# Kernel tuning notes

Hardware: AMD Instinct MI355X
Metric: run time of the kernel (lower is better)

The kernel has to match this reference:

```python
import jax, jax.numpy as jnp
import numpy as np

VOCAB = 30000
FEAT = 30000
HID = 1024
EMB = 1024
B, LQ, LKV = 32, 256, 256


def setup_inputs() -> dict:
    key = jax.random.key(0)
    ks = jax.random.split(key, 8)
    captions = jax.random.randint(ks[0], (B, LKV), 0, VOCAB)
    targets_feature = jax.random.randint(ks[1], (B, LKV), 0, FEAT)
    hidden_state = jax.random.normal(ks[2], (B, LQ, HID), dtype=jnp.float32)
    feature_mask = jax.random.uniform(ks[3], (B, LQ, LKV), dtype=jnp.float32)
    # embeddings initialized uniform(-0.1, 0.1) per init_weights
    Wa = jax.random.uniform(ks[4], (VOCAB, HID), minval=-0.1, maxval=0.1, dtype=jnp.float32)
    Wc = jax.random.uniform(ks[5], (FEAT, HID), minval=-0.1, maxval=0.1, dtype=jnp.float32)
    r = np.sqrt(6.0) / np.sqrt(2 * HID + EMB)
    fc_w = jax.random.uniform(ks[6], (EMB, 2 * HID), minval=-r, maxval=r, dtype=jnp.float32)
    fc_b = jnp.zeros((EMB,), dtype=jnp.float32)
    return {"captions": captions, "hidden_state": hidden_state,
            "targets_feature": targets_feature, "feature_mask": feature_mask,
            "Wa": Wa, "Wc": Wc, "fc_w": fc_w, "fc_b": fc_b}


def reference(captions, hidden_state, targets_feature, feature_mask, Wa, Wc, fc_w, fc_b):
    ea = Wa[captions]           # [B, LKV, H]
    ec = Wc[targets_feature]    # [B, LKV, H]
    # u = hidden_state @ embedding_a^T : [B, LQ, LKV]
    u = jnp.einsum('bqh,bkh->bqk', hidden_state, ea)
    mask = jnp.clip(feature_mask, 0.0, 1.0)
    delta = jnp.exp(u) * mask
    p = delta / (jnp.sum(delta, axis=2, keepdims=True) + 1e-10)  # masked softmax-like weights
    # weighted value sum without materializing [B,LQ,LKV,H] broadcasts
    o = jnp.einsum('bqk,bkh->bqh', p, ec)
    o = jnp.concatenate([hidden_state, o], axis=2)               # [B, LQ, 2H]
    o = o @ fc_w.T + fc_b                                        # [B, LQ, EMB]
    o = o + 1e-10
    norm = jnp.sqrt(jnp.sum(o * o, axis=-1, keepdims=True)) + 1e-8
    return o / norm
```

## Files before the change

### kernel.cpp

```cpp
#include <hip/hip_runtime.h>
#include <hip/hip_bf16.h>

typedef __attribute__((ext_vector_type(8))) short short8;
typedef __attribute__((ext_vector_type(4))) float f32x4;
using bf16 = __hip_bfloat16;


__device__ __forceinline__ void glds16(const void* g, void* lds) {
  __builtin_amdgcn_global_load_lds(
      (const __attribute__((address_space(1))) void*)g,
      (__attribute__((address_space(3))) void*)lds, 16, 0, 0);
}

__global__ __launch_bounds__(256) void k1_prep(
    const int* __restrict__ captions, const float* __restrict__ Wa,
    const float* __restrict__ H, const float* __restrict__ fcw,
    const int* __restrict__ targets, const float* __restrict__ Wc,
    bf16* __restrict__ EA, bf16* __restrict__ X, bf16* __restrict__ FW,
    bf16* __restrict__ ECT) {
  __shared__ float T[64][67];
  int task = blockIdx.x;
  int tid = threadIdx.x;
  if (task < 17408) {
    const float* src;
    bf16* dst;
    int n;
    if (task < 8192) {
      src = Wa + (size_t)captions[task] * 1024;
      dst = EA + (size_t)task * 1024;
      n = 1024;
    } else if (task < 16384) {
      int t = task - 8192;
      src = H + (size_t)t * 1024;
      dst = X + (size_t)t * 2048;
      n = 1024;
    } else {
      int t = task - 16384;
      src = fcw + (size_t)t * 2048;
      dst = FW + (size_t)t * 2048;
      n = 2048;
    }
    for (int c = tid * 4; c < n; c += 1024) {
      float4 v = *(const float4*)(src + c);
      __hip_bfloat162 p0, p1;
      p0.x = __float2bfloat16(v.x); p0.y = __float2bfloat16(v.y);
      p1.x = __float2bfloat16(v.z); p1.y = __float2bfloat16(v.w);
      *(__hip_bfloat162*)(dst + c) = p0;
      *(__hip_bfloat162*)(dst + c + 2) = p1;
    }
    return;
  }
  int bid = task - 17408;
  int b = bid >> 6;
  int kt = (bid >> 4) & 3;
  int ht = bid & 15;
#pragma unroll
  for (int p = 0; p < 4; ++p) {
    int k = p * 16 + (tid >> 4);
    int idx = targets[b * 256 + kt * 64 + k];
    const float* s = Wc + (size_t)idx * 1024 + ht * 64 + (tid & 15) * 4;
    float4 v = *(const float4*)s;
    int c = (tid & 15) * 4;
    T[k][c] = v.x; T[k][c + 1] = v.y; T[k][c + 2] = v.z; T[k][c + 3] = v.w;
  }
  __syncthreads();
#pragma unroll
  for (int p = 0; p < 8; ++p) {
    int h = p * 8 + (tid >> 5);
    int k = (tid & 31) * 2;
    __hip_bfloat162 o;
    o.x = __float2bfloat16(T[k][h]);
    o.y = __float2bfloat16(T[k + 1][h]);
    *(__hip_bfloat162*)(ECT + ((size_t)b * 1024 + ht * 64 + h) * 256 + kt * 64 + k) = o;
  }
}

__global__ __launch_bounds__(256) void k2_scores_softmax(
    const bf16* __restrict__ X, const bf16* __restrict__ EA,
    const float* __restrict__ mask, bf16* __restrict__ P) {
  __shared__ __align__(16) bf16 As[64 * 64];
  __shared__ __align__(16) bf16 Bs[256 * 64];
  int p = blockIdx.x;
  int wg = (p & 7) * 16 + (p >> 3);
  int b = wg >> 2;
  int mb = wg & 3;
  int tid = threadIdx.x;
  int w = tid >> 6, l = tid & 63;
  f32x4 acc[16];
  f32x4 zero = {0.f, 0.f, 0.f, 0.f};
#pragma unroll
  for (int n = 0; n < 16; ++n) acc[n] = zero;

  const bf16* Ag = X + ((size_t)b * 256 + mb * 64) * 2048;
  const bf16* Bg = EA + (size_t)b * 256 * 1024;

  for (int kt = 0; kt < 16; ++kt) {
#pragma unroll
    for (int i = 0; i < 2; ++i) {
      int c = i * 256 + tid;
      int row = c >> 3, slot = c & 7;
      int ss = slot ^ (row & 7);
      glds16(Ag + (size_t)row * 2048 + kt * 64 + ss * 8,
             As + (size_t)(i * 256 + w * 64) * 8);
    }
#pragma unroll
    for (int i = 0; i < 8; ++i) {
      int c = i * 256 + tid;
      int row = c >> 3, slot = c & 7;
      int ss = slot ^ (row & 7);
      glds16(Bg + (size_t)row * 1024 + kt * 64 + ss * 8,
             Bs + (size_t)(i * 256 + w * 64) * 8);
    }
    __syncthreads();
#pragma unroll
    for (int kk = 0; kk < 2; ++kk) {
      int arow = w * 16 + (l & 15);
      int aslot = kk * 4 + (l >> 4);
      short8 af = *(const short8*)(As + arow * 64 + ((aslot ^ (arow & 7)) * 8));
#pragma unroll
      for (int n = 0; n < 16; ++n) {
        int brow = n * 16 + (l & 15);
        int bslot = kk * 4 + (l >> 4);
        short8 bfr = *(const short8*)(Bs + brow * 64 + ((bslot ^ (brow & 7)) * 8));
        acc[n] = __builtin_amdgcn_mfma_f32_16x16x32_bf16(af, bfr, acc[n], 0, 0, 0);
      }
    }
    __syncthreads();
  }
  int q0 = mb * 64 + w * 16 + ((l >> 4) << 2);
  const float* mrow = mask + ((size_t)b * 256 + q0) * 256;
  float s[4] = {0.f, 0.f, 0.f, 0.f};
#pragma unroll
  for (int n = 0; n < 16; ++n) {
    int col = (l & 15) + 16 * n;
#pragma unroll
    for (int i = 0; i < 4; ++i) {
      float mv = mrow[i * 256 + col];
      mv = fminf(fmaxf(mv, 0.f), 1.f);
      float ev = expf(acc[n][i]) * mv;
      acc[n][i] = ev;
      s[i] += ev;
    }
  }
#pragma unroll
  for (int m = 1; m < 16; m <<= 1) {
#pragma unroll
    for (int i = 0; i < 4; ++i) s[i] += __shfl_xor(s[i], m, 64);
  }
  bf16* Prow = P + ((size_t)b * 256 + q0) * 256;
#pragma unroll
  for (int i = 0; i < 4; ++i) {
    float inv = 1.f / (s[i] + 1e-10f);
#pragma unroll
    for (int n = 0; n < 16; ++n) {
      int col = (l & 15) + 16 * n;
      Prow[i * 256 + col] = __float2bfloat16(acc[n][i] * inv);
    }
  }
}

__global__ __launch_bounds__(256) void k3_pv(
    const bf16* __restrict__ P, const bf16* __restrict__ ECT,
    bf16* __restrict__ X) {
  __shared__ __align__(16) bf16 As[128 * 64];
  __shared__ __align__(16) bf16 Bs[128 * 64];
  int p = blockIdx.x;
  int wg = (p & 7) * 64 + (p >> 3);
  int b = wg >> 4;
  int mb = (wg >> 3) & 1;
  int nb = wg & 7;
  int tid = threadIdx.x, w = tid >> 6, l = tid & 63;
  int wr = w >> 1, wc = w & 1;
  f32x4 acc[4][4];
  f32x4 zero = {0.f, 0.f, 0.f, 0.f};
#pragma unroll
  for (int m = 0; m < 4; ++m)
#pragma unroll
    for (int n = 0; n < 4; ++n) acc[m][n] = zero;
  const bf16* Ag = P + (size_t)b * 256 * 256 + mb * 128 * 256;
  const bf16* Bg = ECT + (size_t)b * 1024 * 256 + nb * 128 * 256;
  for (int kt = 0; kt < 4; ++kt) {
#pragma unroll
    for (int i = 0; i < 4; ++i) {
      int c = i * 256 + tid;
      int row = c >> 3, slot = c & 7, ss = slot ^ (row & 7);
      glds16(Ag + (size_t)row * 256 + kt * 64 + ss * 8,
             As + (size_t)(i * 256 + w * 64) * 8);
    }
#pragma unroll
    for (int i = 0; i < 4; ++i) {
      int c = i * 256 + tid;
      int row = c >> 3, slot = c & 7, ss = slot ^ (row & 7);
      glds16(Bg + (size_t)row * 256 + kt * 64 + ss * 8,
             Bs + (size_t)(i * 256 + w * 64) * 8);
    }
    __syncthreads();
#pragma unroll
    for (int kk = 0; kk < 2; ++kk) {
      short8 a[4], bb[4];
#pragma unroll
      for (int m = 0; m < 4; ++m) {
        int row = wr * 64 + m * 16 + (l & 15);
        int slot = kk * 4 + (l >> 4);
        a[m] = *(const short8*)(As + row * 64 + ((slot ^ (row & 7)) * 8));
      }
#pragma unroll
      for (int n = 0; n < 4; ++n) {
        int row = wc * 64 + n * 16 + (l & 15);
        int slot = kk * 4 + (l >> 4);
        bb[n] = *(const short8*)(Bs + row * 64 + ((slot ^ (row & 7)) * 8));
      }
#pragma unroll
      for (int m = 0; m < 4; ++m)
#pragma unroll
        for (int n = 0; n < 4; ++n)
          acc[m][n] = __builtin_amdgcn_mfma_f32_16x16x32_bf16(a[m], bb[n], acc[m][n], 0, 0, 0);
    }
    __syncthreads();
  }
#pragma unroll
  for (int m = 0; m < 4; ++m) {
    int rbase = b * 256 + mb * 128 + wr * 64 + m * 16 + ((l >> 4) << 2);
#pragma unroll
    for (int n = 0; n < 4; ++n) {
      int col = 1024 + nb * 128 + wc * 64 + n * 16 + (l & 15);
#pragma unroll
      for (int i = 0; i < 4; ++i)
        X[(size_t)(rbase + i) * 2048 + col] = __float2bfloat16(acc[m][n][i]);
    }
  }
}

#define K4A (256 * 64)
#define K4B (128 * 64)

__device__ __forceinline__ void k4_stage(const bf16* __restrict__ Ag,
                                         const bf16* __restrict__ Bg, int kt,
                                         bf16* As, bf16* Bs, int tid, int w) {
#pragma unroll
  for (int i = 0; i < 4; ++i) {
    int c = i * 512 + tid;
    int row = c >> 3, ss = (c & 7) ^ (row & 7);
    glds16(Ag + (size_t)row * 2048 + kt * 64 + ss * 8,
           As + (size_t)(i * 512 + w * 64) * 8);
  }
#pragma unroll
  for (int i = 0; i < 2; ++i) {
    int c = i * 512 + tid;
    int row = c >> 3, ss = (c & 7) ^ (row & 7);
    glds16(Bg + (size_t)row * 2048 + kt * 64 + ss * 8,
           Bs + (size_t)(i * 512 + w * 64) * 8);
  }
}

__device__ __forceinline__ void k4_tile(const bf16* As, const bf16* Bs,
                                        int wr, int wc, int l,
                                        f32x4 (&acc)[4][4]) {
  short8 a[2][4], b[2][4];
#pragma unroll
  for (int kk = 0; kk < 2; ++kk)
#pragma unroll
    for (int n = 0; n < 4; ++n) {
      int row = wc * 64 + n * 16 + (l & 15);
      int slot = kk * 4 + (l >> 4);
      b[kk][n] = *(const short8*)(Bs + row * 64 + ((slot ^ (row & 7)) * 8));
    }
#pragma unroll
  for (int kk = 0; kk < 2; ++kk)
#pragma unroll
    for (int m = 0; m < 4; ++m) {
      int row = wr * 64 + m * 16 + (l & 15);
      int slot = kk * 4 + (l >> 4);
      a[kk][m] = *(const short8*)(As + row * 64 + ((slot ^ (row & 7)) * 8));
    }
  __builtin_amdgcn_s_setprio(1);
#pragma unroll
  for (int kk = 0; kk < 2; ++kk)
#pragma unroll
    for (int m = 0; m < 4; ++m)
#pragma unroll
      for (int n = 0; n < 4; ++n)
        acc[m][n] = __builtin_amdgcn_mfma_f32_16x16x32_bf16(
            a[kk][m], b[kk][n], acc[m][n], 0, 0, 0);
  __builtin_amdgcn_s_setprio(0);
}

__global__ __launch_bounds__(512, 1) void k4_fc(
    const bf16* __restrict__ X, const bf16* __restrict__ FW,
    const float* __restrict__ fcb, float* __restrict__ out) {
  __shared__ __align__(16) bf16 As[2][K4A];
  __shared__ __align__(16) bf16 Bs[2][K4B];
  int p = blockIdx.x;
  int wg = (p & 7) * 32 + (p >> 3);
  int mb = wg >> 3;
  int nb = wg & 7;
  int tid = threadIdx.x, w = tid >> 6, l = tid & 63;
  int wr = w >> 1, wc = w & 1;
  f32x4 acc[4][4];
  f32x4 zero = {0.f, 0.f, 0.f, 0.f};
#pragma unroll
  for (int m = 0; m < 4; ++m)
#pragma unroll
    for (int n = 0; n < 4; ++n) acc[m][n] = zero;

  const bf16* Ag = X + (size_t)mb * 256 * 2048;
  const bf16* Bg = FW + (size_t)nb * 128 * 2048;

  k4_stage(Ag, Bg, 0, As[0], Bs[0], tid, w);
  __syncthreads();
  for (int t = 0; t < 32; ++t) {
    int cur = t & 1;
    if (t < 31)
      k4_stage(Ag, Bg, t + 1, As[cur ^ 1], Bs[cur ^ 1], tid, w);
    k4_tile(As[cur], Bs[cur], wr, wc, l, acc);
    __syncthreads();
  }

  float bias[4];
#pragma unroll
  for (int n = 0; n < 4; ++n)
    bias[n] = fcb[nb * 128 + wc * 64 + n * 16 + (l & 15)];
#pragma unroll
  for (int m = 0; m < 4; ++m) {
    int rbase = mb * 256 + wr * 64 + m * 16 + ((l >> 4) << 2);
#pragma unroll
    for (int n = 0; n < 4; ++n) {
      int col = nb * 128 + wc * 64 + n * 16 + (l & 15);
#pragma unroll
      for (int i = 0; i < 4; ++i)
        out[(size_t)(rbase + i) * 1024 + col] = acc[m][n][i] + bias[n] + 1e-10f;
    }
  }
}

__global__ __launch_bounds__(256) void k5_norm(float* __restrict__ y) {
  __shared__ float red[4];
  int row = blockIdx.x;
  float* p = y + (size_t)row * 1024;
  int tid = threadIdx.x;
  float4 v = *(const float4*)(p + tid * 4);
  float ss = v.x * v.x + v.y * v.y + v.z * v.z + v.w * v.w;
#pragma unroll
  for (int m = 1; m < 64; m <<= 1) ss += __shfl_xor(ss, m, 64);
  if ((tid & 63) == 0) red[tid >> 6] = ss;
  __syncthreads();
  float tot = red[0] + red[1] + red[2] + red[3];
  float inv = 1.f / (sqrtf(tot) + 1e-8f);
  float4 o;
  o.x = v.x * inv; o.y = v.y * inv; o.z = v.z * inv; o.w = v.w * inv;
  *(float4*)(p + tid * 4) = o;
}

extern "C" void kernel_launch(void* const* d_in, const int* in_sizes, int n_in,
                              void* d_out, int out_size, void* d_ws, size_t ws_size,
                              hipStream_t stream) {
  const int* captions = (const int*)d_in[0];
  const float* H = (const float*)d_in[1];
  const int* targets = (const int*)d_in[2];
  const float* mask = (const float*)d_in[3];
  const float* Wa = (const float*)d_in[4];
  const float* Wc = (const float*)d_in[5];
  const float* fcw = (const float*)d_in[6];
  const float* fcb = (const float*)d_in[7];
  float* out = (float*)d_out;

  char* ws = (char*)d_ws;
  bf16* EA = (bf16*)(ws);
  bf16* ECT = (bf16*)(ws + (16u << 20));
  bf16* P = (bf16*)(ws + (32u << 20));
  bf16* X = (bf16*)(ws + (36u << 20));
  bf16* FW = (bf16*)(ws + (68u << 20));

  k1_prep<<<19456, 256, 0, stream>>>(captions, Wa, H, fcw, targets, Wc,
                                     EA, X, FW, ECT);
  k2_scores_softmax<<<128, 256, 0, stream>>>(X, EA, mask, P);
  k3_pv<<<512, 256, 0, stream>>>(P, ECT, X);
  k4_fc<<<256, 512, 0, stream>>>(X, FW, fcb, out);
  k5_norm<<<8192, 256, 0, stream>>>(out);
}
```

Before: 128.7 us.

## Fuse scores/softmax and PV kernels, keeping P in LDS

Merges the score+softmax kernel and the P@V kernel into one kernel. Each block handles 32 query rows of one batch, computes the scores, reduces the softmax sums across waves through LDS, and keeps P in swizzled LDS instead of writing it to global memory. It then streams ECT through a double-buffered 128KB LDS region to compute the output. This removes the P round trip and one launch, but each block must reload the full ECT for its batch. At one block per CU, occupancy drops and the EA loads are duplicated across more blocks.

```diff
diff --git a/kernel.cpp b/kernel.cpp
--- a/kernel.cpp
+++ b/kernel.cpp
@@ -75,159 +75,183 @@
   }
 }
 
-__global__ __launch_bounds__(256) void k2_scores_softmax(
-    const bf16* __restrict__ X, const bf16* __restrict__ EA,
-    const float* __restrict__ mask, bf16* __restrict__ P) {
-  __shared__ __align__(16) bf16 As[64 * 64];
-  __shared__ __align__(16) bf16 Bs[256 * 64];
+__global__ __launch_bounds__(256, 1) void k23_scores_pv(
+    bf16* __restrict__ X, const bf16* __restrict__ EA,
+    const bf16* __restrict__ ECT, const float* __restrict__ mask) {
+  __shared__ __align__(16) char smem[16 * 1024 + 512 + 128 * 1024];
+  bf16* p_lds = (bf16*)smem;
+  float* red  = (float*)(smem + 16 * 1024);
+  bf16* big   = (bf16*)(smem + 16 * 1024 + 512);
+
   int p = blockIdx.x;
-  int wg = (p & 7) * 16 + (p >> 3);
-  int b = wg >> 2;
-  int mb = wg & 3;
-  int tid = threadIdx.x;
-  int w = tid >> 6, l = tid & 63;
-  f32x4 acc[16];
+  int wg = (p & 7) * 32 + (p >> 3);
+  int b = wg >> 3;
+  int mb = wg & 7;
+  int tid = threadIdx.x, w = tid >> 6, l = tid & 63;
+
+  const bf16* Ag = X + ((size_t)b * 256 + mb * 32) * 2048;
+  const bf16* Bg = EA + (size_t)b * 256 * 1024;
+  bf16* As = big;
+  bf16* Bs = big + 32 * 64;
+
+  f32x4 sacc[2][4];
   f32x4 zero = {0.f, 0.f, 0.f, 0.f};
 #pragma unroll
-  for (int n = 0; n < 16; ++n) acc[n] = zero;
-
-  const bf16* Ag = X + ((size_t)b * 256 + mb * 64) * 2048;
-  const bf16* Bg = EA + (size_t)b * 256 * 1024;
+  for (int m2 = 0; m2 < 2; ++m2)
+#pragma unroll
+    for (int n = 0; n < 4; ++n) sacc[m2][n] = zero;
 
   for (int kt = 0; kt < 16; ++kt) {
-#pragma unroll
-    for (int i = 0; i < 2; ++i) {
-      int c = i * 256 + tid;
-      int row = c >> 3, slot = c & 7;
-      int ss = slot ^ (row & 7);
+    {
+      int row = tid >> 3, ss = (tid & 7) ^ (row & 7);
       glds16(Ag + (size_t)row * 2048 + kt * 64 + ss * 8,
-             As + (size_t)(i * 256 + w * 64) * 8);
+             As + (size_t)w * 64 * 8);
     }
 #pragma unroll
     for (int i = 0; i < 8; ++i) {
       int c = i * 256 + tid;
-      int row = c >> 3, slot = c & 7;
-      int ss = slot ^ (row & 7);
+      int row = c >> 3, ss = (c & 7) ^ (row & 7);
       glds16(Bg + (size_t)row * 1024 + kt * 64 + ss * 8,
              Bs + (size_t)(i * 256 + w * 64) * 8);
     }
     __syncthreads();
 #pragma unroll
     for (int kk = 0; kk < 2; ++kk) {
-      int arow = w * 16 + (l & 15);
-      int aslot = kk * 4 + (l >> 4);
-      short8 af = *(const short8*)(As + arow * 64 + ((aslot ^ (arow & 7)) * 8));
-#pragma unroll
-      for (int n = 0; n < 16; ++n) {
-        int brow = n * 16 + (l & 15);
-        int bslot = kk * 4 + (l >> 4);
-        short8 bfr = *(const short8*)(Bs + brow * 64 + ((bslot ^ (brow & 7)) * 8));
-        acc[n] = __builtin_amdgcn_mfma_f32_16x16x32_bf16(af, bfr, acc[n], 0, 0, 0);
+      short8 a2[2];
+#pragma unroll
+      for (int m2 = 0; m2 < 2; ++m2) {
+        int ar = m2 * 16 + (l & 15);
+        int sl = kk * 4 + (l >> 4);
+        a2[m2] = *(const short8*)(As + ar * 64 + ((sl ^ (ar & 7)) * 8));
+      }
+#pragma unroll
+      for (int n = 0; n < 4; ++n) {
+        int rb = w * 64 + n * 16 + (l & 15);
+        int sl = kk * 4 + (l >> 4);
+        short8 bfr = *(const short8*)(Bs + rb * 64 + ((sl ^ (rb & 7)) * 8));
+#pragma unroll
+        for (int m2 = 0; m2 < 2; ++m2)
+          sacc[m2][n] = __builtin_amdgcn_mfma_f32_16x16x32_bf16(
+              a2[m2], bfr, sacc[m2][n], 0, 0, 0);
       }
     }
     __syncthreads();
   }
-  int q0 = mb * 64 + w * 16 + ((l >> 4) << 2);
-  const float* mrow = mask + ((size_t)b * 256 + q0) * 256;
-  float s[4] = {0.f, 0.f, 0.f, 0.f};
-#pragma unroll
-  for (int n = 0; n < 16; ++n) {
-    int col = (l & 15) + 16 * n;
+
+  const float* mrow = mask + ((size_t)b * 256 + mb * 32) * 256;
+  float s[2][4] = {{0.f, 0.f, 0.f, 0.f}, {0.f, 0.f, 0.f, 0.f}};
+#pragma unroll
+  for (int m2 = 0; m2 < 2; ++m2)
+#pragma unroll
+    for (int n = 0; n < 4; ++n)
+#pragma unroll
+      for (int i = 0; i < 4; ++i) {
+        int r = m2 * 16 + ((l >> 4) << 2) + i;
+        int c = w * 64 + n * 16 + (l & 15);
+        float mv = mrow[r * 256 + c];
+        mv = fminf(fmaxf(mv, 0.f), 1.f);
+        float ev = expf(sacc[m2][n][i]) * mv;
+        sacc[m2][n][i] = ev;
+        s[m2][i] += ev;
+      }
+#pragma unroll
+  for (int msk = 1; msk < 16; msk <<= 1)
+#pragma unroll
+    for (int m2 = 0; m2 < 2; ++m2)
+#pragma unroll
+      for (int i = 0; i < 4; ++i) s[m2][i] += __shfl_xor(s[m2][i], msk, 64);
+  if ((l & 15) == 0) {
+#pragma unroll
+    for (int m2 = 0; m2 < 2; ++m2)
+#pragma unroll
+      for (int i = 0; i < 4; ++i)
+        red[w * 32 + m2 * 16 + ((l >> 4) << 2) + i] = s[m2][i];
+  }
+  __syncthreads();
+  float inv[2][4];
+#pragma unroll
+  for (int m2 = 0; m2 < 2; ++m2)
 #pragma unroll
     for (int i = 0; i < 4; ++i) {
-      float mv = mrow[i * 256 + col];
-      mv = fminf(fmaxf(mv, 0.f), 1.f);
-      float ev = expf(acc[n][i]) * mv;
-      acc[n][i] = ev;
-      s[i] += ev;
-    }
-  }
-#pragma unroll
-  for (int m = 1; m < 16; m <<= 1) {
-#pragma unroll
-    for (int i = 0; i < 4; ++i) s[i] += __shfl_xor(s[i], m, 64);
-  }
-  bf16* Prow = P + ((size_t)b * 256 + q0) * 256;
-#pragma unroll
-  for (int i = 0; i < 4; ++i) {
-    float inv = 1.f / (s[i] + 1e-10f);
-#pragma unroll
-    for (int n = 0; n < 16; ++n) {
-      int col = (l & 15) + 16 * n;
-      Prow[i * 256 + col] = __float2bfloat16(acc[n][i] * inv);
-    }
-  }
-}
-
-__global__ __launch_bounds__(256) void k3_pv(
-    const bf16* __restrict__ P, const bf16* __restrict__ ECT,
-    bf16* __restrict__ X) {
-  __shared__ __align__(16) bf16 As[128 * 64];
-  __shared__ __align__(16) bf16 Bs[128 * 64];
-  int p = blockIdx.x;
-  int wg = (p & 7) * 64 + (p >> 3);
-  int b = wg >> 4;
-  int mb = (wg >> 3) & 1;
-  int nb = wg & 7;
-  int tid = threadIdx.x, w = tid >> 6, l = tid & 63;
-  int wr = w >> 1, wc = w & 1;
-  f32x4 acc[4][4];
-  f32x4 zero = {0.f, 0.f, 0.f, 0.f};
-#pragma unroll
-  for (int m = 0; m < 4; ++m)
-#pragma unroll
-    for (int n = 0; n < 4; ++n) acc[m][n] = zero;
-  const bf16* Ag = P + (size_t)b * 256 * 256 + mb * 128 * 256;
-  const bf16* Bg = ECT + (size_t)b * 1024 * 256 + nb * 128 * 256;
-  for (int kt = 0; kt < 4; ++kt) {
-#pragma unroll
-    for (int i = 0; i < 4; ++i) {
-      int c = i * 256 + tid;
-      int row = c >> 3, slot = c & 7, ss = slot ^ (row & 7);
-      glds16(Ag + (size_t)row * 256 + kt * 64 + ss * 8,
-             As + (size_t)(i * 256 + w * 64) * 8);
-    }
-#pragma unroll
-    for (int i = 0; i < 4; ++i) {
-      int c = i * 256 + tid;
-      int row = c >> 3, slot = c & 7, ss = slot ^ (row & 7);
-      glds16(Bg + (size_t)row * 256 + kt * 64 + ss * 8,
-             Bs + (size_t)(i * 256 + w * 64) * 8);
+      int r = m2 * 16 + ((l >> 4) << 2) + i;
+      float tot = red[r] + red[32 + r] + red[64 + r] + red[96 + r];
+      inv[m2][i] = 1.f / (tot + 1e-10f);
+    }
+#pragma unroll
+  for (int m2 = 0; m2 < 2; ++m2)
+#pragma unroll
+    for (int n = 0; n < 4; ++n)
+#pragma unroll
+      for (int i = 0; i < 4; ++i) {
+        int r = m2 * 16 + ((l >> 4) << 2) + i;
+        int c = w * 64 + n * 16 + (l & 15);
+        float pv = sacc[m2][n][i] * inv[m2][i];
+        p_lds[r * 256 + (((c >> 3) ^ (r & 7)) << 3) + (c & 7)] =
+            __float2bfloat16(pv);
+      }
+  __syncthreads();
+
+  bf16* XO = X + ((size_t)b * 256 + mb * 32) * 2048 + 1024;
+  for (int np = 0; np < 2; ++np) {
+    f32x4 acc[2][8];
+#pragma unroll
+    for (int m2 = 0; m2 < 2; ++m2)
+#pragma unroll
+      for (int n = 0; n < 8; ++n) acc[m2][n] = zero;
+
+#pragma unroll
+    for (int it = 0; it < 16; ++it) {
+      int g = it * 64 + l;
+      int row = g >> 3, ss = (g & 7) ^ (row & 7);
+      glds16(ECT + ((size_t)b * 1024 + np * 512 + w * 128 + row) * 256 + ss * 8,
+             big + (size_t)(0 * 4 + w) * 8192 + (size_t)it * 512);
     }
     __syncthreads();
-#pragma unroll
-    for (int kk = 0; kk < 2; ++kk) {
-      short8 a[4], bb[4];
-#pragma unroll
-      for (int m = 0; m < 4; ++m) {
-        int row = wr * 64 + m * 16 + (l & 15);
-        int slot = kk * 4 + (l >> 4);
-        a[m] = *(const short8*)(As + row * 64 + ((slot ^ (row & 7)) * 8));
-      }
-#pragma unroll
-      for (int n = 0; n < 4; ++n) {
-        int row = wc * 64 + n * 16 + (l & 15);
-        int slot = kk * 4 + (l >> 4);
-        bb[n] = *(const short8*)(Bs + row * 64 + ((slot ^ (row & 7)) * 8));
-      }
-#pragma unroll
-      for (int m = 0; m < 4; ++m)
-#pragma unroll
-        for (int n = 0; n < 4; ++n)
-          acc[m][n] = __builtin_amdgcn_mfma_f32_16x16x32_bf16(a[m], bb[n], acc[m][n], 0, 0, 0);
-    }
-    __syncthreads();
-  }
-#pragma unroll
-  for (int m = 0; m < 4; ++m) {
-    int rbase = b * 256 + mb * 128 + wr * 64 + m * 16 + ((l >> 4) << 2);
-#pragma unroll
-    for (int n = 0; n < 4; ++n) {
-      int col = 1024 + nb * 128 + wc * 64 + n * 16 + (l & 15);
-#pragma unroll
-      for (int i = 0; i < 4; ++i)
-        X[(size_t)(rbase + i) * 2048 + col] = __float2bfloat16(acc[m][n][i]);
-    }
+    for (int kt = 0; kt < 4; ++kt) {
+      int cur = kt & 1;
+      if (kt < 3) {
+#pragma unroll
+        for (int it = 0; it < 16; ++it) {
+          int g = it * 64 + l;
+          int row = g >> 3, ss = (g & 7) ^ (row & 7);
+          glds16(ECT + ((size_t)b * 1024 + np * 512 + w * 128 + row) * 256 +
+                     (kt + 1) * 64 + ss * 8,
+                 big + (size_t)((cur ^ 1) * 4 + w) * 8192 + (size_t)it * 512);
+        }
+      }
+      const bf16* Bw = big + (size_t)(cur * 4 + w) * 8192;
+#pragma unroll
+      for (int kk = 0; kk < 2; ++kk) {
+        short8 a2[2];
+#pragma unroll
+        for (int m2 = 0; m2 < 2; ++m2) {
+          int ar = m2 * 16 + (l & 15);
+          int sl = kt * 8 + kk * 4 + (l >> 4);
+          a2[m2] = *(const short8*)(p_lds + ar * 256 + ((sl ^ (ar & 7)) * 8));
+        }
+#pragma unroll
+        for (int n = 0; n < 8; ++n) {
+          int rb = n * 16 + (l & 15);
+          int sl = kk * 4 + (l >> 4);
+          short8 bfr = *(const short8*)(Bw + rb * 64 + ((sl ^ (rb & 7)) * 8));
+#pragma unroll
+          for (int m2 = 0; m2 < 2; ++m2)
+            acc[m2][n] = __builtin_amdgcn_mfma_f32_16x16x32_bf16(
+                a2[m2], bfr, acc[m2][n], 0, 0, 0);
+        }
+      }
+      __syncthreads();
+    }
+#pragma unroll
+    for (int m2 = 0; m2 < 2; ++m2)
+#pragma unroll
+      for (int n = 0; n < 8; ++n) {
+        int rl = m2 * 16 + ((l >> 4) << 2);
+        int col = np * 512 + w * 128 + n * 16 + (l & 15);
+#pragma unroll
+        for (int i = 0; i < 4; ++i)
+          XO[(size_t)(rl + i) * 2048 + col] = __float2bfloat16(acc[m2][n][i]);
+      }
   }
 }
 
@@ -367,14 +391,12 @@
   char* ws = (char*)d_ws;
   bf16* EA = (bf16*)(ws);
   bf16* ECT = (bf16*)(ws + (16u << 20));
-  bf16* P = (bf16*)(ws + (32u << 20));
   bf16* X = (bf16*)(ws + (36u << 20));
   bf16* FW = (bf16*)(ws + (68u << 20));
 
   k1_prep<<<19456, 256, 0, stream>>>(captions, Wa, H, fcw, targets, Wc,
                                      EA, X, FW, ECT);
-  k2_scores_softmax<<<128, 256, 0, stream>>>(X, EA, mask, P);
-  k3_pv<<<512, 256, 0, stream>>>(P, ECT, X);
+  k23_scores_pv<<<256, 256, 0, stream>>>(X, EA, ECT, mask);
   k4_fc<<<256, 512, 0, stream>>>(X, FW, fcb, out);
   k5_norm<<<8192, 256, 0, stream>>>(out);
 }
```

New measurement: 118.6 us. -7.8%, faster.
